# Kernel optimization log

Hardware: AMD Instinct MI355X
Metric: run time of the kernel (lower is better)

## Reference

```python
import jax, jax.numpy as jnp
import numpy as np

H_SIZE = 128
E_SIZE = 16
N_LAYERS = 3
N_ATOMS = 80000
N_BLOCKS = 16000
N_EDGES = 320000
N_GRAPHS = 128


def setup_inputs() -> dict:
    key = jax.random.key(0)
    ks = jax.random.split(key, 20)
    p = lambda k, shape: (0.02 * jax.random.normal(k, shape, dtype=jnp.float32))
    h = H_SIZE
    inp = {
        'H': jax.random.normal(ks[0], (N_ATOMS, h), dtype=jnp.float32),
        'Z': jax.random.normal(ks[1], (N_ATOMS, 1, 3), dtype=jnp.float32),
        'block_id': jnp.sort(jax.random.randint(ks[2], (N_ATOMS,), 0, N_BLOCKS)),
        'batch_id': jnp.sort(jax.random.randint(ks[3], (N_BLOCKS,), 0, N_GRAPHS)),
        'edges': jax.random.randint(ks[4], (2, N_EDGES), 0, N_BLOCKS),
        'edge_attr': jax.random.normal(ks[5], (N_EDGES, E_SIZE), dtype=jnp.float32),
        # EGNN parameters
        'emb_in_w': p(ks[6], (h, h)), 'emb_in_b': jnp.zeros((h,), jnp.float32),
        'emb_out_w': p(ks[7], (h, h)), 'emb_out_b': jnp.zeros((h,), jnp.float32),
        'edge_w1': p(ks[8], (N_LAYERS, 2 * h + 1 + E_SIZE, h)), 'edge_b1': jnp.zeros((N_LAYERS, h), jnp.float32),
        'edge_w2': p(ks[9], (N_LAYERS, h, h)), 'edge_b2': jnp.zeros((N_LAYERS, h), jnp.float32),
        'node_w1': p(ks[10], (N_LAYERS, 2 * h, h)), 'node_b1': jnp.zeros((N_LAYERS, h), jnp.float32),
        'node_w2': p(ks[11], (N_LAYERS, h, h)), 'node_b2': jnp.zeros((N_LAYERS, h), jnp.float32),
        'coord_w1': p(ks[12], (N_LAYERS, h, h)), 'coord_b1': jnp.zeros((N_LAYERS, h), jnp.float32),
        'coord_w3': p(ks[13], (N_LAYERS, h, 1)),  # final coord layer, no bias
    }
    return inp


def _normalize(x, eps=1e-12):
    # F.normalize(dim=-1): x / max(||x||_2, eps)
    n = jnp.linalg.norm(x, axis=-1, keepdims=True)
    return x / jnp.maximum(n, eps)


def _seg_mean(x, ids, n):
    s = jax.ops.segment_sum(x, ids, num_segments=n)
    c = jax.ops.segment_sum(jnp.ones((x.shape[0], 1), x.dtype), ids, num_segments=n)
    return s / jnp.maximum(c, 1.0)


def _egnn_forward(H, Z, block_id, batch_id, edges, edge_attr,
                  emb_in_w, emb_in_b, emb_out_w, emb_out_b,
                  edge_w1, edge_b1, edge_w2, edge_b2,
                  node_w1, node_b1, node_w2, node_b2,
                  coord_w1, coord_b1, coord_w3):
    silu = jax.nn.silu
    # atom -> block pooling (scatter_mean)
    Hm = _seg_mean(H, block_id, N_BLOCKS)                      # [B, h]
    x = _seg_mean(Z.reshape(Z.shape[0], -1), block_id, N_BLOCKS)  # [B, 3] (squeeze of [B,1,3])
    row, col = edges[0], edges[1]

    h = Hm @ emb_in_w + emb_in_b
    for l in range(N_LAYERS):
        diff = x[row] - x[col]                                 # [E, 3]
        radial = jnp.sum(diff * diff, axis=-1, keepdims=True)  # [E, 1]
        e_in = jnp.concatenate([h[row], h[col], radial, edge_attr], axis=-1)  # [E, 2h+1+e]
        m = silu(silu(e_in @ edge_w1[l] + edge_b1[l]) @ edge_w2[l] + edge_b2[l])  # edge MLP [E, h]
        # coordinate update: per-edge scalar weight, mean aggregation
        w = silu(m @ coord_w1[l] + coord_b1[l]) @ coord_w3[l]  # [E, 1]
        x = x + _seg_mean(diff * w, row, N_BLOCKS)
        # node update: sum aggregation of messages, residual
        agg = jax.ops.segment_sum(m, row, num_segments=N_BLOCKS)  # [B, h]
        h = h + (silu(jnp.concatenate([h, agg], axis=-1) @ node_w1[l] + node_b1[l]) @ node_w2[l] + node_b2[l])
    h = h @ emb_out_w + emb_out_b

    block_repr = _normalize(h)                                  # [B, h]
    graph_repr = _normalize(jax.ops.segment_sum(block_repr, batch_id, num_segments=N_GRAPHS))  # [G, h]
    return Hm, block_repr, graph_repr


def reference(H, Z, block_id, batch_id, edges, edge_attr,
              emb_in_w, emb_in_b, emb_out_w, emb_out_b,
              edge_w1, edge_b1, edge_w2, edge_b2,
              node_w1, node_b1, node_w2, node_b2,
              coord_w1, coord_b1, coord_w3):
    return _egnn_forward(H, Z, block_id, batch_id, edges, edge_attr,
                         emb_in_w, emb_in_b, emb_out_w, emb_out_b,
                         edge_w1, edge_b1, edge_w2, edge_b2,
                         node_w1, node_b1, node_w2, node_b2,
                         coord_w1, coord_b1, coord_w3)
```

## Files before the change

### kernel.cpp

```cpp
#include <hip/hip_runtime.h>

#define N_ATOMS  80000
#define N_BLOCKS 16000
#define N_EDGES  320000
#define N_GRAPHS 128
#define HS       128

typedef unsigned short ushortT;
typedef __attribute__((ext_vector_type(8))) __bf16 bf16x8;
typedef __attribute__((ext_vector_type(8))) unsigned short ushort8;
typedef __attribute__((ext_vector_type(4))) float f32x4;

__device__ __forceinline__ unsigned short f2bf(float f){
  unsigned int u = __builtin_bit_cast(unsigned int, f);
  u = (u + 0x7FFFu + ((u >> 16) & 1u)) >> 16;
  return (unsigned short)u;
}
__device__ __forceinline__ ushortT f2bff(float f){
  __bf16 b = (__bf16)f;
  return __builtin_bit_cast(ushortT, b);
}
__device__ __forceinline__ float bf2f(ushortT u){
  unsigned int v = ((unsigned int)u) << 16;
  return __builtin_bit_cast(float, v);
}
__device__ __forceinline__ bf16x8 load8bf(const ushortT* p){
  uint4 u = *reinterpret_cast<const uint4*>(p);
  return __builtin_bit_cast(bf16x8, u);
}
__device__ __forceinline__ bf16x8 load8f_bf(const float* p){
  float4 a = *reinterpret_cast<const float4*>(p);
  float4 b = *reinterpret_cast<const float4*>(p + 4);
  ushort8 u = { f2bff(a.x), f2bff(a.y), f2bff(a.z), f2bff(a.w),
                f2bff(b.x), f2bff(b.y), f2bff(b.z), f2bff(b.w) };
  return __builtin_bit_cast(bf16x8, u);
}
__device__ __forceinline__ float silu(float v){
  return v * __builtin_amdgcn_rcpf(1.f + __expf(-v));
}

__device__ __forceinline__ int c_of_p(int p){
  int ks = p >> 5, lg = (p >> 3) & 3, j = p & 7;
  return 16 * (ks * 2 + (j >> 2)) + lg * 4 + (j & 3);
}

struct PrepParams {
  const float* ew1; const float* ew2; const float* cw1;
  const float* nw1; const float* nw2; const float* ei; const float* eo;
  const float* eb1;
  ushortT* W1atp; ushortT* W1btp; ushortT* W1ct; ushortT* W2tp; ushortT* CW1tp;
  ushortT* NW1t; ushortT* NW2t; ushortT* Eint; ushortT* Eoutt;
  float* b1p; int* hist;
};

__device__ __forceinline__ void tcvt(int idx, const float* __restrict__ src,
                                     ushortT* __restrict__ dst,
                                     int srcK, int row_off, int K, int N, int Kpad,
                                     int pn, int pk){
  int k = idx % Kpad;
  int rem = idx / Kpad;
  int n = rem % N;
  int l = rem / N;
  float v = 0.f;
  if (k < K){
    int kk = pk ? c_of_p(k) : k;
    int nn = pn ? c_of_p(n) : n;
    v = src[((size_t)l * srcK + row_off + kk) * N + nn];
  }
  dst[idx] = f2bf(v);
}

#define PREP_TOTAL (49152*5 + 12288 + 98304 + 16384*2 + 16000 + 384)

__global__ void prep_kernel(PrepParams P){
  int idx = blockIdx.x * 256 + threadIdx.x;
  if (idx < 49152){ tcvt(idx, P.ew1, P.W1atp, 273,   0, 128, 128, 128, 1, 0); return; }
  idx -= 49152;
  if (idx < 49152){ tcvt(idx, P.ew1, P.W1btp, 273, 128, 128, 128, 128, 1, 0); return; }
  idx -= 49152;
  if (idx < 12288){ tcvt(idx, P.ew1, P.W1ct,  273, 256,  17, 128,  32, 0, 0); return; }
  idx -= 12288;
  if (idx < 49152){ tcvt(idx, P.ew2, P.W2tp,  128,   0, 128, 128, 128, 0, 1); return; }
  idx -= 49152;
  if (idx < 49152){ tcvt(idx, P.cw1, P.CW1tp, 128,   0, 128, 128, 128, 0, 1); return; }
  idx -= 49152;
  if (idx < 98304){ tcvt(idx, P.nw1, P.NW1t,  256,   0, 256, 128, 256, 0, 0); return; }
  idx -= 98304;
  if (idx < 49152){ tcvt(idx, P.nw2, P.NW2t,  128,   0, 128, 128, 128, 0, 0); return; }
  idx -= 49152;
  if (idx < 16384){ tcvt(idx, P.ei,  P.Eint,  128,   0, 128, 128, 128, 0, 0); return; }
  idx -= 16384;
  if (idx < 16384){ tcvt(idx, P.eo,  P.Eoutt, 128,   0, 128, 128, 128, 0, 0); return; }
  idx -= 16384;
  if (idx < 16000){ P.hist[idx] = 0; return; }
  idx -= 16000;
  if (idx < 384){ int l = idx >> 7, p = idx & 127; P.b1p[idx] = P.eb1[l * 128 + c_of_p(p)]; }
}

__global__ void hist_bstart_kernel(const int* __restrict__ edges, int* __restrict__ hist,
                                   const int* __restrict__ bid, int* __restrict__ bstart){
  int b = blockIdx.x;
  if (b < N_EDGES / 256){
    int e = b * 256 + threadIdx.x;
    atomicAdd(&hist[edges[e]], 1);
  } else {
    int i = (b - N_EDGES / 256) * 256 + threadIdx.x;
    if (i <= N_BLOCKS){
      int lo = 0, hi = N_ATOMS;
      while (lo < hi){ int mid = (lo + hi) >> 1; if (bid[mid] < i) lo = mid + 1; else hi = mid; }
      bstart[i] = lo;
    }
  }
}

__global__ __launch_bounds__(1024) void scan_kernel(const int* __restrict__ hist,
                                                    int* __restrict__ estart,
                                                    int* __restrict__ ecur){
  __shared__ int ps[1024];
  int t = threadIdx.x;
  const int chunk = (N_BLOCKS + 1023) / 1024;
  int lo = t * chunk, hi = lo + chunk;
  if (hi > N_BLOCKS) hi = N_BLOCKS;
  if (lo > N_BLOCKS) lo = N_BLOCKS;
  int s = 0;
  for (int i = lo; i < hi; i++) s += hist[i];
  ps[t] = s;
  __syncthreads();
  for (int off = 1; off < 1024; off <<= 1){
    int v = (t >= off) ? ps[t - off] : 0;
    __syncthreads();
    ps[t] += v;
    __syncthreads();
  }
  int base = (t == 0) ? 0 : ps[t - 1];
  for (int i = lo; i < hi; i++){ estart[i] = base; ecur[i] = base; base += hist[i]; }
  if (t == 1023) estart[N_BLOCKS] = base;
}

__global__ void scatter_kernel(const int* __restrict__ edges, const float* __restrict__ attr,
                               int* __restrict__ ecur,
                               int* __restrict__ srow, int* __restrict__ scol,
                               ushortT* __restrict__ sattr){
  int e = blockIdx.x * 256 + threadIdx.x;
  if (e >= N_EDGES) return;
  int r = edges[e], c = edges[N_EDGES + e];
  int p = atomicAdd(&ecur[r], 1);
  srow[p] = r; scol[p] = c;
  ushortT buf[32];
  buf[0] = 0;
#pragma unroll
  for (int k = 0; k < 16; k++) buf[k + 1] = f2bf(attr[(size_t)e * 16 + k]);
#pragma unroll
  for (int k = 17; k < 32; k++) buf[k] = 0;
#pragma unroll
  for (int k = 0; k < 16; k++)
    reinterpret_cast<uint*>(sattr + (size_t)p * 32)[k] = reinterpret_cast<uint*>(buf)[k];
}

__global__ void pool_kernel(const float* __restrict__ H, const float* __restrict__ Z,
                            const int* __restrict__ start,
                            float* __restrict__ Hm, float* __restrict__ x,
                            float* __restrict__ gsum){
  int b = blockIdx.x;
  int t = threadIdx.x;
  if (b < 128) gsum[b * 128 + t] = 0.f;
  int s = start[b], e = start[b + 1];
  float inv = 1.f / (float)((e - s) > 0 ? (e - s) : 1);
  float sum = 0.f;
  for (int a = s; a < e; a++) sum += H[(size_t)a * HS + t];
  Hm[(size_t)b * HS + t] = sum * inv;
  if (t < 3){
    float sz = 0.f;
    for (int a = s; a < e; a++) sz += Z[a * 3 + t];
    x[b * 3 + t] = sz * inv;
  }
}

__global__ __launch_bounds__(64) void gemm_pq_kernel(
    const float* __restrict__ A,
    const ushortT* __restrict__ Wt, const float* __restrict__ bias,
    float* __restrict__ Cf,
    const ushortT* __restrict__ Wa, const ushortT* __restrict__ Wb,
    const float* __restrict__ b1p,
    ushortT* __restrict__ Pbf, ushortT* __restrict__ Qbf,
    float* __restrict__ agg, float* __restrict__ xacc){
  __shared__ __align__(16) ushortT T1[2048];
  int lane = threadIdx.x;
  int l15 = lane & 15, lg = lane >> 4;
  int base = blockIdx.x * 16;
  int row = base + l15;
  {
    float4 z4 = {0.f, 0.f, 0.f, 0.f};
    float4* aggp = reinterpret_cast<float4*>(agg + (size_t)blockIdx.x * 16 * HS);
#pragma unroll
    for (int i = 0; i < 8; i++) aggp[lane + 64 * i] = z4;
    if (lane < 48) xacc[blockIdx.x * 48 + lane] = 0.f;
  }
  f32x4 zero = {0.f, 0.f, 0.f, 0.f};
  f32x4 acc[8];
#pragma unroll
  for (int n = 0; n < 8; n++) acc[n] = zero;
#pragma unroll
  for (int ks = 0; ks < 4; ks++){
    int k0 = ks * 32 + lg * 8;
    bf16x8 af = load8f_bf(A + (size_t)row * HS + k0);
#pragma unroll
    for (int n = 0; n < 8; n++){
      bf16x8 bf = load8bf(Wt + (size_t)(16 * n + l15) * HS + k0);
      acc[n] = __builtin_amdgcn_mfma_f32_16x16x32_bf16(af, bf, acc[n], 0, 0, 0);
    }
  }
#pragma unroll
  for (int n = 0; n < 8; n++){
    int col = 16 * n + l15;
    float bv = bias[col];
#pragma unroll
    for (int r = 0; r < 4; r++){
      int ro = base + lg * 4 + r;
      int er = lg * 4 + r;
      float hv = acc[n][r] + bv;
      Cf[(size_t)ro * HS + col] = hv;
      T1[(er * 128 + col) ^ ((er & 7) << 3)] = f2bff(hv);
    }
  }
  f32x4 accp[8], accq[8];
#pragma unroll
  for (int n = 0; n < 8; n++){ accp[n] = zero; accq[n] = zero; }
#pragma unroll
  for (int ks = 0; ks < 4; ks++){
    int k0 = ks * 32 + lg * 8;
    bf16x8 af = load8bf(&T1[(l15 * 128 + k0) ^ ((l15 & 7) << 3)]);
#pragma unroll
    for (int n = 0; n < 8; n++){
      accp[n] = __builtin_amdgcn_mfma_f32_16x16x32_bf16(af, load8bf(Wa + (size_t)(16 * n + l15) * HS + k0), accp[n], 0, 0, 0);
      accq[n] = __builtin_amdgcn_mfma_f32_16x16x32_bf16(af, load8bf(Wb + (size_t)(16 * n + l15) * HS + k0), accq[n], 0, 0, 0);
    }
  }
#pragma unroll
  for (int n = 0; n < 8; n++){
    int col = 16 * n + l15;
    float bv = b1p[col];
#pragma unroll
    for (int r = 0; r < 4; r++){
      int ro = base + lg * 4 + r;
      Pbf[(size_t)ro * HS + col] = f2bff(accp[n][r] + bv);
      Qbf[(size_t)ro * HS + col] = f2bff(accq[n][r]);
    }
  }
}

__global__ __launch_bounds__(64) void node_pq_kernel(
    float* __restrict__ h, float* __restrict__ agg,
    const ushortT* __restrict__ W1t, const ushortT* __restrict__ W2t,
    const float* __restrict__ b1, const float* __restrict__ b2,
    const ushortT* __restrict__ Wa, const ushortT* __restrict__ Wb,
    const float* __restrict__ b1p,
    ushortT* __restrict__ Pbf, ushortT* __restrict__ Qbf,
    float* __restrict__ x, float* __restrict__ xacc, const int* __restrict__ estart){
  __shared__ __align__(16) ushortT T1[2048];
  int lane = threadIdx.x;
  int l15 = lane & 15, lg = lane >> 4;
  int base = blockIdx.x * 16;
  int row = base + l15;
  f32x4 zero = {0.f, 0.f, 0.f, 0.f};

  if (lane < 48){
    int i = blockIdx.x * 48 + lane;
    int b = i / 3;
    int cnt = estart[b + 1] - estart[b];
    x[i] += xacc[i] / (float)(cnt > 0 ? cnt : 1);
    xacc[i] = 0.f;
  }

  f32x4 acc[8];
#pragma unroll
  for (int n = 0; n < 8; n++) acc[n] = zero;
#pragma unroll
  for (int ks = 0; ks < 8; ks++){
    int k0 = ks * 32 + lg * 8;
    bf16x8 af = (k0 < 128) ? load8f_bf(h + (size_t)row * HS + k0)
                           : load8f_bf(agg + (size_t)row * HS + (k0 - 128));
#pragma unroll
    for (int n = 0; n < 8; n++){
      acc[n] = __builtin_amdgcn_mfma_f32_16x16x32_bf16(af, load8bf(W1t + (size_t)(16 * n + l15) * 256 + k0), acc[n], 0, 0, 0);
    }
  }
  __syncthreads();
  {
    float4 z4 = {0.f, 0.f, 0.f, 0.f};
    float4* aggp = reinterpret_cast<float4*>(agg + (size_t)blockIdx.x * 16 * HS);
#pragma unroll
    for (int i = 0; i < 8; i++) aggp[lane + 64 * i] = z4;
  }
#pragma unroll
  for (int n = 0; n < 8; n++){
    int col = 16 * n + l15;
    float bv = b1[col];
#pragma unroll
    for (int r = 0; r < 4; r++){
      int er = lg * 4 + r;
      T1[(er * 128 + col) ^ ((er & 7) << 3)] = f2bff(silu(acc[n][r] + bv));
    }
  }
#pragma unroll
  for (int n = 0; n < 8; n++) acc[n] = zero;
#pragma unroll
  for (int ks = 0; ks < 4; ks++){
    int k0 = ks * 32 + lg * 8;
    bf16x8 af = load8bf(&T1[(l15 * 128 + k0) ^ ((l15 & 7) << 3)]);
#pragma unroll
    for (int n = 0; n < 8; n++){
      acc[n] = __builtin_amdgcn_mfma_f32_16x16x32_bf16(af, load8bf(W2t + (size_t)(16 * n + l15) * HS + k0), acc[n], 0, 0, 0);
    }
  }
#pragma unroll
  for (int n = 0; n < 8; n++){
    int col = 16 * n + l15;
    float bv = b2[col];
#pragma unroll
    for (int r = 0; r < 4; r++){
      int ro = base + lg * 4 + r;
      int er = lg * 4 + r;
      float hv = h[(size_t)ro * HS + col] + acc[n][r] + bv;
      h[(size_t)ro * HS + col] = hv;
      T1[(er * 128 + col) ^ ((er & 7) << 3)] = f2bff(hv);
    }
  }
  f32x4 accp[8], accq[8];
#pragma unroll
  for (int n = 0; n < 8; n++){ accp[n] = zero; accq[n] = zero; }
#pragma unroll
  for (int ks = 0; ks < 4; ks++){
    int k0 = ks * 32 + lg * 8;
    bf16x8 af = load8bf(&T1[(l15 * 128 + k0) ^ ((l15 & 7) << 3)]);
#pragma unroll
    for (int n = 0; n < 8; n++){
      accp[n] = __builtin_amdgcn_mfma_f32_16x16x32_bf16(af, load8bf(Wa + (size_t)(16 * n + l15) * HS + k0), accp[n], 0, 0, 0);
      accq[n] = __builtin_amdgcn_mfma_f32_16x16x32_bf16(af, load8bf(Wb + (size_t)(16 * n + l15) * HS + k0), accq[n], 0, 0, 0);
    }
  }
#pragma unroll
  for (int n = 0; n < 8; n++){
    int col = 16 * n + l15;
    float bv = b1p[col];
#pragma unroll
    for (int r = 0; r < 4; r++){
      int ro = base + lg * 4 + r;
      Pbf[(size_t)ro * HS + col] = f2bff(accp[n][r] + bv);
      Qbf[(size_t)ro * HS + col] = f2bff(accq[n][r]);
    }
  }
}

__global__ __launch_bounds__(64) void node_emb_kernel(
    const float* __restrict__ h, const float* __restrict__ agg,
    const ushortT* __restrict__ W1t, const ushortT* __restrict__ W2t,
    const float* __restrict__ b1, const float* __restrict__ b2,
    const ushortT* __restrict__ Eoutt, const float* __restrict__ eob,
    const int* __restrict__ batch_id,
    float* __restrict__ brep, float* __restrict__ gsum){
  __shared__ __align__(16) ushortT T1[2048];
  int lane = threadIdx.x;
  int l15 = lane & 15, lg = lane >> 4;
  int base = blockIdx.x * 16;
  int row = base + l15;
  f32x4 zero = {0.f, 0.f, 0.f, 0.f};

  f32x4 acc[8];
#pragma unroll
  for (int n = 0; n < 8; n++) acc[n] = zero;
#pragma unroll
  for (int ks = 0; ks < 8; ks++){
    int k0 = ks * 32 + lg * 8;
    bf16x8 af = (k0 < 128) ? load8f_bf(h + (size_t)row * HS + k0)
                           : load8f_bf(agg + (size_t)row * HS + (k0 - 128));
#pragma unroll
    for (int n = 0; n < 8; n++){
      acc[n] = __builtin_amdgcn_mfma_f32_16x16x32_bf16(af, load8bf(W1t + (size_t)(16 * n + l15) * 256 + k0), acc[n], 0, 0, 0);
    }
  }
#pragma unroll
  for (int n = 0; n < 8; n++){
    int col = 16 * n + l15;
    float bv = b1[col];
#pragma unroll
    for (int r = 0; r < 4; r++){
      int er = lg * 4 + r;
      T1[(er * 128 + col) ^ ((er & 7) << 3)] = f2bff(silu(acc[n][r] + bv));
    }
  }
#pragma unroll
  for (int n = 0; n < 8; n++) acc[n] = zero;
#pragma unroll
  for (int ks = 0; ks < 4; ks++){
    int k0 = ks * 32 + lg * 8;
    bf16x8 af = load8bf(&T1[(l15 * 128 + k0) ^ ((l15 & 7) << 3)]);
#pragma unroll
    for (int n = 0; n < 8; n++){
      acc[n] = __builtin_amdgcn_mfma_f32_16x16x32_bf16(af, load8bf(W2t + (size_t)(16 * n + l15) * HS + k0), acc[n], 0, 0, 0);
    }
  }
#pragma unroll
  for (int n = 0; n < 8; n++){
    int col = 16 * n + l15;
    float bv = b2[col];
#pragma unroll
    for (int r = 0; r < 4; r++){
      int ro = base + lg * 4 + r;
      int er = lg * 4 + r;
      float hv = h[(size_t)ro * HS + col] + acc[n][r] + bv;
      T1[(er * 128 + col) ^ ((er & 7) << 3)] = f2bff(hv);
    }
  }
#pragma unroll
  for (int n = 0; n < 8; n++) acc[n] = zero;
#pragma unroll
  for (int ks = 0; ks < 4; ks++){
    int k0 = ks * 32 + lg * 8;
    bf16x8 af = load8bf(&T1[(l15 * 128 + k0) ^ ((l15 & 7) << 3)]);
#pragma unroll
    for (int n = 0; n < 8; n++){
      acc[n] = __builtin_amdgcn_mfma_f32_16x16x32_bf16(af, load8bf(Eoutt + (size_t)(16 * n + l15) * HS + k0), acc[n], 0, 0, 0);
    }
  }
#pragma unroll
  for (int n = 0; n < 8; n++){
    float bv = eob[16 * n + l15];
#pragma unroll
    for (int r = 0; r < 4; r++) acc[n][r] += bv;
  }
  float scl[4];
#pragma unroll
  for (int r = 0; r < 4; r++){
    float ss = 0.f;
#pragma unroll
    for (int n = 0; n < 8; n++) ss += acc[n][r] * acc[n][r];
#pragma unroll
    for (int o = 1; o < 16; o <<= 1) ss += __shfl_xor(ss, o, 64);
    scl[r] = 1.f / fmaxf(sqrtf(ss), 1e-12f);
  }
#pragma unroll
  for (int r = 0; r < 4; r++){
    int ro = base + lg * 4 + r;
    int g = batch_id[ro];
#pragma unroll
    for (int n = 0; n < 8; n++){
      int col = 16 * n + l15;
      float v = acc[n][r] * scl[r];
      brep[(size_t)ro * HS + col] = v;
      atomicAdd(&gsum[g * HS + col], v);
    }
  }
}

template<int COORD>
__global__ __launch_bounds__(256, 4) void edge_kernel(
    const int* __restrict__ srow, const int* __restrict__ scol,
    const ushortT* __restrict__ sattr,
    const float* __restrict__ x,
    const ushortT* __restrict__ Pbf, const ushortT* __restrict__ Qbf,
    const ushortT* __restrict__ W1ct, const ushortT* __restrict__ W2tp,
    const ushortT* __restrict__ CW1tp,
    const float* __restrict__ b2, const float* __restrict__ cb1,
    const float* __restrict__ cw3,
    float* __restrict__ xacc, float* __restrict__ agg){
  __shared__ float bias_l[3][128];
  __shared__ int   rid_s[64];
  __shared__ float dif_s[COORD ? 64 : 1][3];
  __shared__ float wall[COORD ? 4 : 1][COORD ? 64 : 1];
  __shared__ __align__(16) ushortT S1[64 * 128];
  __shared__ __align__(16) ushortT S2[64 * 128];

  const int t = threadIdx.x;
  const int lane = t & 63;
  const int wv = t >> 6;
  const int l15 = lane & 15, lg = lane >> 4;
  const f32x4 zero = {0.f, 0.f, 0.f, 0.f};

  if (t < 128){
    bias_l[0][t] = b2[t];
    if (COORD){ bias_l[1][t] = cb1[t]; bias_l[2][t] = cw3[t]; }
  }

  const int erow = wv * 16 + l15;
  const int e = blockIdx.x * 64 + erow;
  const int r = srow[e], c = scol[e];
  const float dx = x[r * 3 + 0] - x[c * 3 + 0];
  const float dy = x[r * 3 + 1] - x[c * 3 + 1];
  const float dz = x[r * 3 + 2] - x[c * 3 + 2];
  const float rad = dx * dx + dy * dy + dz * dz;
  if (lg == 0){
    rid_s[erow] = r;
    if (COORD){ dif_s[erow][0] = dx; dif_s[erow][1] = dy; dif_s[erow][2] = dz; }
  }
  ushort8 at8 = __builtin_bit_cast(ushort8, load8bf(sattr + (size_t)e * 32 + lg * 8));
  if (lg == 0) at8[0] = f2bff(rad);
  const bf16x8 atb = __builtin_bit_cast(bf16x8, at8);

#pragma unroll
  for (int ks = 0; ks < 4; ks++){
    f32x4 a0 = __builtin_amdgcn_mfma_f32_16x16x32_bf16(
        load8bf(W1ct + (size_t)(16 * (2 * ks)     + l15) * 32 + lg * 8), atb, zero, 0, 0, 0);
    f32x4 a1 = __builtin_amdgcn_mfma_f32_16x16x32_bf16(
        load8bf(W1ct + (size_t)(16 * (2 * ks + 1) + l15) * 32 + lg * 8), atb, zero, 0, 0, 0);
    ushort8 pv = __builtin_bit_cast(ushort8, load8bf(Pbf + (size_t)r * HS + ks * 32 + lg * 8));
    ushort8 qv = __builtin_bit_cast(ushort8, load8bf(Qbf + (size_t)c * HS + ks * 32 + lg * 8));
    ushort8 af;
#pragma unroll
    for (int j = 0; j < 4; j++)
      af[j] = f2bff(silu(a0[j] + bf2f(pv[j]) + bf2f(qv[j])));
#pragma unroll
    for (int j = 4; j < 8; j++)
      af[j] = f2bff(silu(a1[j - 4] + bf2f(pv[j]) + bf2f(qv[j])));
    int byte = (erow * 256 + ks * 64 + lg * 16) ^ ((erow & 7) << 4);
    *reinterpret_cast<uint4*>(reinterpret_cast<char*>(S1) + byte) = __builtin_bit_cast(uint4, af);
  }
  __syncthreads();

  f32x4 acc2[4][2];
#pragma unroll
  for (int et = 0; et < 4; et++){ acc2[et][0] = zero; acc2[et][1] = zero; }
#pragma unroll
  for (int ks = 0; ks < 4; ks++){
    bf16x8 wf0 = load8bf(W2tp + (size_t)(16 * (2 * wv)     + l15) * HS + ks * 32 + lg * 8);
    bf16x8 wf1 = load8bf(W2tp + (size_t)(16 * (2 * wv + 1) + l15) * HS + ks * 32 + lg * 8);
#pragma unroll
    for (int et = 0; et < 4; et++){
      int row2 = et * 16 + l15;
      int byte = (row2 * 256 + ks * 64 + lg * 16) ^ ((row2 & 7) << 4);
      bf16x8 mb = __builtin_bit_cast(bf16x8,
          *reinterpret_cast<const uint4*>(reinterpret_cast<const char*>(S1) + byte));
      acc2[et][0] = __builtin_amdgcn_mfma_f32_16x16x32_bf16(wf0, mb, acc2[et][0], 0, 0, 0);
      acc2[et][1] = __builtin_amdgcn_mfma_f32_16x16x32_bf16(wf1, mb, acc2[et][1], 0, 0, 0);
    }
  }
  ushort8 mreg[4];
#pragma unroll
  for (int et = 0; et < 4; et++){
    ushort8 mq;
#pragma unroll
    for (int g = 0; g < 2; g++){
      float4 bv = *reinterpret_cast<const float4*>(&bias_l[0][16 * (2 * wv + g) + lg * 4]);
#pragma unroll
      for (int rr = 0; rr < 4; rr++)
        mq[g * 4 + rr] = f2bff(silu(acc2[et][g][rr] + (&bv.x)[rr]));
    }
    mreg[et] = mq;
    int row2 = et * 16 + l15;
    int byte = (row2 * 256 + wv * 64 + lg * 16) ^ ((row2 & 7) << 4);
    *reinterpret_cast<uint4*>(reinterpret_cast<char*>(S2) + byte) = __builtin_bit_cast(uint4, mq);
  }
  __syncthreads();

  if (COORD){
    f32x4 acc3[4][2];
#pragma unroll
    for (int et = 0; et < 4; et++){ acc3[et][0] = zero; acc3[et][1] = zero; }
#pragma unroll
    for (int ks = 0; ks < 4; ks++){
      bf16x8 wf0 = load8bf(CW1tp + (size_t)(16 * (2 * wv)     + l15) * HS + ks * 32 + lg * 8);
      bf16x8 wf1 = load8bf(CW1tp + (size_t)(16 * (2 * wv + 1) + l15) * HS + ks * 32 + lg * 8);
#pragma unroll
      for (int et = 0; et < 4; et++){
        bf16x8 mb;
        if (ks == wv){
          mb = __builtin_bit_cast(bf16x8, mreg[et]);
        } else {
          int row2 = et * 16 + l15;
          int byte = (row2 * 256 + ks * 64 + lg * 16) ^ ((row2 & 7) << 4);
          mb = __builtin_bit_cast(bf16x8,
              *reinterpret_cast<const uint4*>(reinterpret_cast<const char*>(S2) + byte));
        }
        acc3[et][0] = __builtin_amdgcn_mfma_f32_16x16x32_bf16(wf0, mb, acc3[et][0], 0, 0, 0);
        acc3[et][1] = __builtin_amdgcn_mfma_f32_16x16x32_bf16(wf1, mb, acc3[et][1], 0, 0, 0);
      }
    }
#pragma unroll
    for (int et = 0; et < 4; et++){
      float ws = 0.f;
#pragma unroll
      for (int g = 0; g < 2; g++){
        int n = 2 * wv + g;
        float4 cbv = *reinterpret_cast<const float4*>(&bias_l[1][16 * n + lg * 4]);
        float4 cwv = *reinterpret_cast<const float4*>(&bias_l[2][16 * n + lg * 4]);
#pragma unroll
        for (int rr = 0; rr < 4; rr++)
          ws += silu(acc3[et][g][rr] + (&cbv.x)[rr]) * (&cwv.x)[rr];
      }
      ws += __shfl_xor(ws, 16, 64);
      ws += __shfl_xor(ws, 32, 64);
      if (lg == 0) wall[wv][et * 16 + l15] = ws;
    }
  }

  {
    const int c0 = c_of_p(2 * lane), c1 = c_of_p(2 * lane + 1);
    float run0 = 0.f, run1 = 0.f;
    int prev = __builtin_amdgcn_readfirstlane(rid_s[wv * 16]);
#pragma unroll
    for (int e2 = 0; e2 < 16; e2++){
      int re = __builtin_amdgcn_readfirstlane(rid_s[wv * 16 + e2]);
      if (re != prev){
        atomicAdd(&agg[(size_t)prev * HS + c0], run0);
        atomicAdd(&agg[(size_t)prev * HS + c1], run1);
        run0 = 0.f; run1 = 0.f; prev = re;
      }
      int row2 = wv * 16 + e2;
      int byte = (row2 * 256 + lane * 4) ^ ((row2 & 7) << 4);
      uint u = *reinterpret_cast<const uint*>(reinterpret_cast<const char*>(S2) + byte);
      run0 += bf2f((ushortT)(u & 0xFFFF));
      run1 += bf2f((ushortT)(u >> 16));
    }
    atomicAdd(&agg[(size_t)prev * HS + c0], run0);
    atomicAdd(&agg[(size_t)prev * HS + c1], run1);
  }

  if (COORD){
    __syncthreads();
    if (t < 192){
      int e2 = t / 3, cd = t % 3;
      float w = wall[0][e2] + wall[1][e2] + wall[2][e2] + wall[3][e2];
      atomicAdd(&xacc[(size_t)rid_s[e2] * 3 + cd], dif_s[e2][cd] * w);
    }
  }
}

__global__ void norm_graph_kernel(const float* __restrict__ gsum, float* __restrict__ grep){
  int wv = threadIdx.x >> 6, lane = threadIdx.x & 63;
  int g = blockIdx.x * 4 + wv;
  if (g >= N_GRAPHS) return;
  float v0 = gsum[g * HS + lane];
  float v1 = gsum[g * HS + 64 + lane];
  float ss = v0 * v0 + v1 * v1;
#pragma unroll
  for (int o = 1; o < 64; o <<= 1) ss += __shfl_xor(ss, o, 64);
  float s = 1.f / fmaxf(sqrtf(ss), 1e-12f);
  grep[(size_t)g * HS + lane] = v0 * s;
  grep[(size_t)g * HS + 64 + lane] = v1 * s;
}

extern "C" void kernel_launch(void* const* d_in, const int* in_sizes, int n_in,
                              void* d_out, int out_size, void* d_ws, size_t ws_size,
                              hipStream_t stream){
  const float* H         = (const float*)d_in[0];
  const float* Z         = (const float*)d_in[1];
  const int*   block_id  = (const int*)d_in[2];
  const int*   batch_id  = (const int*)d_in[3];
  const int*   edges     = (const int*)d_in[4];
  const float* edge_attr = (const float*)d_in[5];
  const float* emb_in_w  = (const float*)d_in[6];
  const float* emb_in_b  = (const float*)d_in[7];
  const float* emb_out_w = (const float*)d_in[8];
  const float* emb_out_b = (const float*)d_in[9];
  const float* edge_w1   = (const float*)d_in[10];
  const float* edge_b1   = (const float*)d_in[11];
  const float* edge_w2   = (const float*)d_in[12];
  const float* edge_b2   = (const float*)d_in[13];
  const float* node_w1   = (const float*)d_in[14];
  const float* node_b1   = (const float*)d_in[15];
  const float* node_w2   = (const float*)d_in[16];
  const float* node_b2   = (const float*)d_in[17];
  const float* coord_w1  = (const float*)d_in[18];
  const float* coord_b1  = (const float*)d_in[19];
  const float* coord_w3  = (const float*)d_in[20];

  float* out  = (float*)d_out;
  float* Hm   = out;
  float* brep = out + (size_t)N_BLOCKS * HS;
  float* grep = out + (size_t)2 * N_BLOCKS * HS;

  char* base = (char*)d_ws;
  size_t off = 0;
  auto take = [&](size_t bytes) -> char* {
    char* p = base + off;
    off += (bytes + 255) & ~(size_t)255;
    return p;
  };
  float*   x     = (float*)  take((size_t)N_BLOCKS * 3 * 4);
  float*   xacc  = (float*)  take((size_t)N_BLOCKS * 3 * 4);
  float*   h     = (float*)  take((size_t)N_BLOCKS * HS * 4);
  float*   agg   = (float*)  take((size_t)N_BLOCKS * HS * 4);
  float*   gsum  = (float*)  take((size_t)N_GRAPHS * HS * 4);
  int*     bstart= (int*)    take((size_t)(N_BLOCKS + 1) * 4);
  int*     hist  = (int*)    take((size_t)N_BLOCKS * 4);
  int*     estart= (int*)    take((size_t)(N_BLOCKS + 1) * 4);
  int*     ecur  = (int*)    take((size_t)N_BLOCKS * 4);
  int*     srow  = (int*)    take((size_t)N_EDGES * 4);
  int*     scol  = (int*)    take((size_t)N_EDGES * 4);
  ushortT* sattr = (ushortT*)take((size_t)N_EDGES * 32 * 2);
  ushortT* Pbf   = (ushortT*)take((size_t)N_BLOCKS * HS * 2);
  ushortT* Qbf   = (ushortT*)take((size_t)N_BLOCKS * HS * 2);
  ushortT* W1atp = (ushortT*)take((size_t)3 * 128 * 128 * 2);
  ushortT* W1btp = (ushortT*)take((size_t)3 * 128 * 128 * 2);
  ushortT* W1ct  = (ushortT*)take((size_t)3 * 128 * 32 * 2);
  ushortT* W2tp  = (ushortT*)take((size_t)3 * 128 * 128 * 2);
  ushortT* CW1tp = (ushortT*)take((size_t)3 * 128 * 128 * 2);
  ushortT* NW1t  = (ushortT*)take((size_t)3 * 128 * 256 * 2);
  ushortT* NW2t  = (ushortT*)take((size_t)3 * 128 * 128 * 2);
  ushortT* Eint  = (ushortT*)take((size_t)128 * 128 * 2);
  ushortT* Eoutt = (ushortT*)take((size_t)128 * 128 * 2);
  float*   b1p   = (float*)  take((size_t)3 * 128 * 4);

  PrepParams P;
  P.ew1 = edge_w1; P.ew2 = edge_w2; P.cw1 = coord_w1;
  P.nw1 = node_w1; P.nw2 = node_w2; P.ei = emb_in_w; P.eo = emb_out_w;
  P.eb1 = edge_b1;
  P.W1atp = W1atp; P.W1btp = W1btp; P.W1ct = W1ct; P.W2tp = W2tp; P.CW1tp = CW1tp;
  P.NW1t = NW1t; P.NW2t = NW2t; P.Eint = Eint; P.Eoutt = Eoutt;
  P.b1p = b1p; P.hist = hist;
  prep_kernel<<<(PREP_TOTAL + 255) / 256, 256, 0, stream>>>(P);

  hist_bstart_kernel<<<N_EDGES / 256 + (N_BLOCKS + 1 + 255) / 256, 256, 0, stream>>>(
      edges, hist, block_id, bstart);
  scan_kernel<<<1, 1024, 0, stream>>>(hist, estart, ecur);
  scatter_kernel<<<N_EDGES / 256, 256, 0, stream>>>(edges, edge_attr, ecur, srow, scol, sattr);
  pool_kernel<<<N_BLOCKS, 128, 0, stream>>>(H, Z, bstart, Hm, x, gsum);

  gemm_pq_kernel<<<N_BLOCKS / 16, 64, 0, stream>>>(Hm, Eint, emb_in_b, h,
                                                   W1atp, W1btp, b1p, Pbf, Qbf, agg, xacc);

  for (int l = 0; l < 3; l++){
    if (l < 2){
      edge_kernel<1><<<N_EDGES / 64, 256, 0, stream>>>(
          srow, scol, sattr, x, Pbf, Qbf,
          W1ct + (size_t)l * 128 * 32, W2tp + (size_t)l * 128 * 128, CW1tp + (size_t)l * 128 * 128,
          edge_b2 + l * 128, coord_b1 + l * 128, coord_w3 + l * 128,
          xacc, agg);
      node_pq_kernel<<<N_BLOCKS / 16, 64, 0, stream>>>(
          h, agg, NW1t + (size_t)l * 128 * 256, NW2t + (size_t)l * 128 * 128,
          node_b1 + l * 128, node_b2 + l * 128,
          W1atp + (size_t)(l + 1) * 128 * 128, W1btp + (size_t)(l + 1) * 128 * 128,
          b1p + (l + 1) * 128, Pbf, Qbf, x, xacc, estart);
    } else {
      edge_kernel<0><<<N_EDGES / 64, 256, 0, stream>>>(
          srow, scol, sattr, x, Pbf, Qbf,
          W1ct + (size_t)l * 128 * 32, W2tp + (size_t)l * 128 * 128, CW1tp + (size_t)l * 128 * 128,
          edge_b2 + l * 128, coord_b1 + l * 128, coord_w3 + l * 128,
          xacc, agg);
      node_emb_kernel<<<N_BLOCKS / 16, 64, 0, stream>>>(
          h, agg, NW1t + (size_t)l * 128 * 256, NW2t + (size_t)l * 128 * 128,
          node_b1 + l * 128, node_b2 + l * 128,
          Eoutt, emb_out_b, batch_id, brep, gsum);
    }
  }

  norm_graph_kernel<<<N_GRAPHS / 4, 256, 0, stream>>>(gsum, grep);
}
```

Measured before the change: 521.5 us.

## Process two edge tiles per block, reusing weight fragments in registers

```diff
diff --git a/kernel.cpp b/kernel.cpp
--- a/kernel.cpp
+++ b/kernel.cpp
@@ -454,7 +454,7 @@
 }
 
 template<int COORD>
-__global__ __launch_bounds__(256, 4) void edge_kernel(
+__global__ __launch_bounds__(256, 3) void edge_kernel(
     const int* __restrict__ srow, const int* __restrict__ scol,
     const ushortT* __restrict__ sattr,
     const float* __restrict__ x,
@@ -482,146 +482,162 @@
     if (COORD){ bias_l[1][t] = cb1[t]; bias_l[2][t] = cw3[t]; }
   }
 
+  bf16x8 wf2[4][2];
+  bf16x8 cwf[4][2];
+  const int c0 = c_of_p(2 * lane), c1 = c_of_p(2 * lane + 1);
+  float run0 = 0.f, run1 = 0.f;
+  int prev = -1;
+
   const int erow = wv * 16 + l15;
-  const int e = blockIdx.x * 64 + erow;
-  const int r = srow[e], c = scol[e];
-  const float dx = x[r * 3 + 0] - x[c * 3 + 0];
-  const float dy = x[r * 3 + 1] - x[c * 3 + 1];
-  const float dz = x[r * 3 + 2] - x[c * 3 + 2];
-  const float rad = dx * dx + dy * dy + dz * dz;
-  if (lg == 0){
-    rid_s[erow] = r;
-    if (COORD){ dif_s[erow][0] = dx; dif_s[erow][1] = dy; dif_s[erow][2] = dz; }
-  }
-  ushort8 at8 = __builtin_bit_cast(ushort8, load8bf(sattr + (size_t)e * 32 + lg * 8));
-  if (lg == 0) at8[0] = f2bff(rad);
-  const bf16x8 atb = __builtin_bit_cast(bf16x8, at8);
-
-#pragma unroll
-  for (int ks = 0; ks < 4; ks++){
-    f32x4 a0 = __builtin_amdgcn_mfma_f32_16x16x32_bf16(
-        load8bf(W1ct + (size_t)(16 * (2 * ks)     + l15) * 32 + lg * 8), atb, zero, 0, 0, 0);
-    f32x4 a1 = __builtin_amdgcn_mfma_f32_16x16x32_bf16(
-        load8bf(W1ct + (size_t)(16 * (2 * ks + 1) + l15) * 32 + lg * 8), atb, zero, 0, 0, 0);
-    ushort8 pv = __builtin_bit_cast(ushort8, load8bf(Pbf + (size_t)r * HS + ks * 32 + lg * 8));
-    ushort8 qv = __builtin_bit_cast(ushort8, load8bf(Qbf + (size_t)c * HS + ks * 32 + lg * 8));
-    ushort8 af;
-#pragma unroll
-    for (int j = 0; j < 4; j++)
-      af[j] = f2bff(silu(a0[j] + bf2f(pv[j]) + bf2f(qv[j])));
-#pragma unroll
-    for (int j = 4; j < 8; j++)
-      af[j] = f2bff(silu(a1[j - 4] + bf2f(pv[j]) + bf2f(qv[j])));
-    int byte = (erow * 256 + ks * 64 + lg * 16) ^ ((erow & 7) << 4);
-    *reinterpret_cast<uint4*>(reinterpret_cast<char*>(S1) + byte) = __builtin_bit_cast(uint4, af);
-  }
-  __syncthreads();
-
-  f32x4 acc2[4][2];
-#pragma unroll
-  for (int et = 0; et < 4; et++){ acc2[et][0] = zero; acc2[et][1] = zero; }
-#pragma unroll
-  for (int ks = 0; ks < 4; ks++){
-    bf16x8 wf0 = load8bf(W2tp + (size_t)(16 * (2 * wv)     + l15) * HS + ks * 32 + lg * 8);
-    bf16x8 wf1 = load8bf(W2tp + (size_t)(16 * (2 * wv + 1) + l15) * HS + ks * 32 + lg * 8);
+
+#pragma unroll
+  for (int tile = 0; tile < 2; tile++){
+    const int e = blockIdx.x * 128 + tile * 64 + erow;
+    const int r = srow[e], c = scol[e];
+    const float dx = x[r * 3 + 0] - x[c * 3 + 0];
+    const float dy = x[r * 3 + 1] - x[c * 3 + 1];
+    const float dz = x[r * 3 + 2] - x[c * 3 + 2];
+    const float rad = dx * dx + dy * dy + dz * dz;
+    ushort8 at8 = __builtin_bit_cast(ushort8, load8bf(sattr + (size_t)e * 32 + lg * 8));
+    if (lg == 0) at8[0] = f2bff(rad);
+    const bf16x8 atb = __builtin_bit_cast(bf16x8, at8);
+
+#pragma unroll
+    for (int ks = 0; ks < 4; ks++){
+      f32x4 a0 = __builtin_amdgcn_mfma_f32_16x16x32_bf16(
+          load8bf(W1ct + (size_t)(16 * (2 * ks)     + l15) * 32 + lg * 8), atb, zero, 0, 0, 0);
+      f32x4 a1 = __builtin_amdgcn_mfma_f32_16x16x32_bf16(
+          load8bf(W1ct + (size_t)(16 * (2 * ks + 1) + l15) * 32 + lg * 8), atb, zero, 0, 0, 0);
+      ushort8 pv = __builtin_bit_cast(ushort8, load8bf(Pbf + (size_t)r * HS + ks * 32 + lg * 8));
+      ushort8 qv = __builtin_bit_cast(ushort8, load8bf(Qbf + (size_t)c * HS + ks * 32 + lg * 8));
+      ushort8 af;
+#pragma unroll
+      for (int j = 0; j < 4; j++)
+        af[j] = f2bff(silu(a0[j] + bf2f(pv[j]) + bf2f(qv[j])));
+#pragma unroll
+      for (int j = 4; j < 8; j++)
+        af[j] = f2bff(silu(a1[j - 4] + bf2f(pv[j]) + bf2f(qv[j])));
+      int byte = (erow * 256 + ks * 64 + lg * 16) ^ ((erow & 7) << 4);
+      *reinterpret_cast<uint4*>(reinterpret_cast<char*>(S1) + byte) = __builtin_bit_cast(uint4, af);
+    }
+    __syncthreads();
+
+    if (lg == 0){
+      rid_s[erow] = r;
+      if (COORD){ dif_s[erow][0] = dx; dif_s[erow][1] = dy; dif_s[erow][2] = dz; }
+    }
+
+    f32x4 acc2[4][2];
+#pragma unroll
+    for (int et = 0; et < 4; et++){ acc2[et][0] = zero; acc2[et][1] = zero; }
+#pragma unroll
+    for (int ks = 0; ks < 4; ks++){
+      if (tile == 0){
+        wf2[ks][0] = load8bf(W2tp + (size_t)(16 * (2 * wv)     + l15) * HS + ks * 32 + lg * 8);
+        wf2[ks][1] = load8bf(W2tp + (size_t)(16 * (2 * wv + 1) + l15) * HS + ks * 32 + lg * 8);
+      }
+#pragma unroll
+      for (int et = 0; et < 4; et++){
+        int row2 = et * 16 + l15;
+        int byte = (row2 * 256 + ks * 64 + lg * 16) ^ ((row2 & 7) << 4);
+        bf16x8 mb = __builtin_bit_cast(bf16x8,
+            *reinterpret_cast<const uint4*>(reinterpret_cast<const char*>(S1) + byte));
+        acc2[et][0] = __builtin_amdgcn_mfma_f32_16x16x32_bf16(wf2[ks][0], mb, acc2[et][0], 0, 0, 0);
+        acc2[et][1] = __builtin_amdgcn_mfma_f32_16x16x32_bf16(wf2[ks][1], mb, acc2[et][1], 0, 0, 0);
+      }
+    }
+    ushort8 mreg[4];
 #pragma unroll
     for (int et = 0; et < 4; et++){
+      ushort8 mq;
+#pragma unroll
+      for (int g = 0; g < 2; g++){
+        float4 bv = *reinterpret_cast<const float4*>(&bias_l[0][16 * (2 * wv + g) + lg * 4]);
+#pragma unroll
+        for (int rr = 0; rr < 4; rr++)
+          mq[g * 4 + rr] = f2bff(silu(acc2[et][g][rr] + (&bv.x)[rr]));
+      }
+      mreg[et] = mq;
       int row2 = et * 16 + l15;
-      int byte = (row2 * 256 + ks * 64 + lg * 16) ^ ((row2 & 7) << 4);
-      bf16x8 mb = __builtin_bit_cast(bf16x8,
-          *reinterpret_cast<const uint4*>(reinterpret_cast<const char*>(S1) + byte));
-      acc2[et][0] = __builtin_amdgcn_mfma_f32_16x16x32_bf16(wf0, mb, acc2[et][0], 0, 0, 0);
-      acc2[et][1] = __builtin_amdgcn_mfma_f32_16x16x32_bf16(wf1, mb, acc2[et][1], 0, 0, 0);
-    }
-  }
-  ushort8 mreg[4];
-#pragma unroll
-  for (int et = 0; et < 4; et++){
-    ushort8 mq;
-#pragma unroll
-    for (int g = 0; g < 2; g++){
-      float4 bv = *reinterpret_cast<const float4*>(&bias_l[0][16 * (2 * wv + g) + lg * 4]);
-#pragma unroll
-      for (int rr = 0; rr < 4; rr++)
-        mq[g * 4 + rr] = f2bff(silu(acc2[et][g][rr] + (&bv.x)[rr]));
-    }
-    mreg[et] = mq;
-    int row2 = et * 16 + l15;
-    int byte = (row2 * 256 + wv * 64 + lg * 16) ^ ((row2 & 7) << 4);
-    *reinterpret_cast<uint4*>(reinterpret_cast<char*>(S2) + byte) = __builtin_bit_cast(uint4, mq);
-  }
-  __syncthreads();
-
-  if (COORD){
-    f32x4 acc3[4][2];
-#pragma unroll
-    for (int et = 0; et < 4; et++){ acc3[et][0] = zero; acc3[et][1] = zero; }
-#pragma unroll
-    for (int ks = 0; ks < 4; ks++){
-      bf16x8 wf0 = load8bf(CW1tp + (size_t)(16 * (2 * wv)     + l15) * HS + ks * 32 + lg * 8);
-      bf16x8 wf1 = load8bf(CW1tp + (size_t)(16 * (2 * wv + 1) + l15) * HS + ks * 32 + lg * 8);
+      int byte = (row2 * 256 + wv * 64 + lg * 16) ^ ((row2 & 7) << 4);
+      *reinterpret_cast<uint4*>(reinterpret_cast<char*>(S2) + byte) = __builtin_bit_cast(uint4, mq);
+    }
+    __syncthreads();
+
+    if (COORD){
+      f32x4 acc3[4][2];
+#pragma unroll
+      for (int et = 0; et < 4; et++){ acc3[et][0] = zero; acc3[et][1] = zero; }
+#pragma unroll
+      for (int ks = 0; ks < 4; ks++){
+        if (tile == 0){
+          cwf[ks][0] = load8bf(CW1tp + (size_t)(16 * (2 * wv)     + l15) * HS + ks * 32 + lg * 8);
+          cwf[ks][1] = load8bf(CW1tp + (size_t)(16 * (2 * wv + 1) + l15) * HS + ks * 32 + lg * 8);
+        }
+#pragma unroll
+        for (int et = 0; et < 4; et++){
+          bf16x8 mb;
+          if (ks == wv){
+            mb = __builtin_bit_cast(bf16x8, mreg[et]);
+          } else {
+            int row2 = et * 16 + l15;
+            int byte = (row2 * 256 + ks * 64 + lg * 16) ^ ((row2 & 7) << 4);
+            mb = __builtin_bit_cast(bf16x8,
+                *reinterpret_cast<const uint4*>(reinterpret_cast<const char*>(S2) + byte));
+          }
+          acc3[et][0] = __builtin_amdgcn_mfma_f32_16x16x32_bf16(cwf[ks][0], mb, acc3[et][0], 0, 0, 0);
+          acc3[et][1] = __builtin_amdgcn_mfma_f32_16x16x32_bf16(cwf[ks][1], mb, acc3[et][1], 0, 0, 0);
+        }
+      }
 #pragma unroll
       for (int et = 0; et < 4; et++){
-        bf16x8 mb;
-        if (ks == wv){
-          mb = __builtin_bit_cast(bf16x8, mreg[et]);
-        } else {
-          int row2 = et * 16 + l15;
-          int byte = (row2 * 256 + ks * 64 + lg * 16) ^ ((row2 & 7) << 4);
-          mb = __builtin_bit_cast(bf16x8,
-              *reinterpret_cast<const uint4*>(reinterpret_cast<const char*>(S2) + byte));
+        float ws = 0.f;
+#pragma unroll
+        for (int g = 0; g < 2; g++){
+          int n = 2 * wv + g;
+          float4 cbv = *reinterpret_cast<const float4*>(&bias_l[1][16 * n + lg * 4]);
+          float4 cwv = *reinterpret_cast<const float4*>(&bias_l[2][16 * n + lg * 4]);
+#pragma unroll
+          for (int rr = 0; rr < 4; rr++)
+            ws += silu(acc3[et][g][rr] + (&cbv.x)[rr]) * (&cwv.x)[rr];
         }
-        acc3[et][0] = __builtin_amdgcn_mfma_f32_16x16x32_bf16(wf0, mb, acc3[et][0], 0, 0, 0);
-        acc3[et][1] = __builtin_amdgcn_mfma_f32_16x16x32_bf16(wf1, mb, acc3[et][1], 0, 0, 0);
+        ws += __shfl_xor(ws, 16, 64);
+        ws += __shfl_xor(ws, 32, 64);
+        if (lg == 0) wall[wv][et * 16 + l15] = ws;
       }
     }
-#pragma unroll
-    for (int et = 0; et < 4; et++){
-      float ws = 0.f;
-#pragma unroll
-      for (int g = 0; g < 2; g++){
-        int n = 2 * wv + g;
-        float4 cbv = *reinterpret_cast<const float4*>(&bias_l[1][16 * n + lg * 4]);
-        float4 cwv = *reinterpret_cast<const float4*>(&bias_l[2][16 * n + lg * 4]);
-#pragma unroll
-        for (int rr = 0; rr < 4; rr++)
-          ws += silu(acc3[et][g][rr] + (&cbv.x)[rr]) * (&cwv.x)[rr];
+
+    {
+#pragma unroll
+      for (int e2 = 0; e2 < 16; e2++){
+        int re = __builtin_amdgcn_readfirstlane(rid_s[wv * 16 + e2]);
+        if (re != prev){
+          if (prev >= 0){
+            atomicAdd(&agg[(size_t)prev * HS + c0], run0);
+            atomicAdd(&agg[(size_t)prev * HS + c1], run1);
+          }
+          run0 = 0.f; run1 = 0.f; prev = re;
+        }
+        int row2 = wv * 16 + e2;
+        int byte = (row2 * 256 + lane * 4) ^ ((row2 & 7) << 4);
+        uint u = *reinterpret_cast<const uint*>(reinterpret_cast<const char*>(S2) + byte);
+        run0 += bf2f((ushortT)(u & 0xFFFF));
+        run1 += bf2f((ushortT)(u >> 16));
       }
-      ws += __shfl_xor(ws, 16, 64);
-      ws += __shfl_xor(ws, 32, 64);
-      if (lg == 0) wall[wv][et * 16 + l15] = ws;
-    }
-  }
-
-  {
-    const int c0 = c_of_p(2 * lane), c1 = c_of_p(2 * lane + 1);
-    float run0 = 0.f, run1 = 0.f;
-    int prev = __builtin_amdgcn_readfirstlane(rid_s[wv * 16]);
-#pragma unroll
-    for (int e2 = 0; e2 < 16; e2++){
-      int re = __builtin_amdgcn_readfirstlane(rid_s[wv * 16 + e2]);
-      if (re != prev){
-        atomicAdd(&agg[(size_t)prev * HS + c0], run0);
-        atomicAdd(&agg[(size_t)prev * HS + c1], run1);
-        run0 = 0.f; run1 = 0.f; prev = re;
+    }
+
+    if (COORD){
+      __syncthreads();
+      if (t < 192){
+        int e2 = t / 3, cd = t % 3;
+        float w = wall[0][e2] + wall[1][e2] + wall[2][e2] + wall[3][e2];
+        atomicAdd(&xacc[(size_t)rid_s[e2] * 3 + cd], dif_s[e2][cd] * w);
       }
-      int row2 = wv * 16 + e2;
-      int byte = (row2 * 256 + lane * 4) ^ ((row2 & 7) << 4);
-      uint u = *reinterpret_cast<const uint*>(reinterpret_cast<const char*>(S2) + byte);
-      run0 += bf2f((ushortT)(u & 0xFFFF));
-      run1 += bf2f((ushortT)(u >> 16));
-    }
+    }
+  }
+  if (prev >= 0){
     atomicAdd(&agg[(size_t)prev * HS + c0], run0);
     atomicAdd(&agg[(size_t)prev * HS + c1], run1);
-  }
-
-  if (COORD){
-    __syncthreads();
-    if (t < 192){
-      int e2 = t / 3, cd = t % 3;
-      float w = wall[0][e2] + wall[1][e2] + wall[2][e2] + wall[3][e2];
-      atomicAdd(&xacc[(size_t)rid_s[e2] * 3 + cd], dif_s[e2][cd] * w);
-    }
   }
 }
 
@@ -721,7 +737,7 @@
 
   for (int l = 0; l < 3; l++){
     if (l < 2){
-      edge_kernel<1><<<N_EDGES / 64, 256, 0, stream>>>(
+      edge_kernel<1><<<N_EDGES / 128, 256, 0, stream>>>(
           srow, scol, sattr, x, Pbf, Qbf,
           W1ct + (size_t)l * 128 * 32, W2tp + (size_t)l * 128 * 128, CW1tp + (size_t)l * 128 * 128,
           edge_b2 + l * 128, coord_b1 + l * 128, coord_w3 + l * 128,
@@ -732,7 +748,7 @@
           W1atp + (size_t)(l + 1) * 128 * 128, W1btp + (size_t)(l + 1) * 128 * 128,
           b1p + (l + 1) * 128, Pbf, Qbf, x, xacc, estart);
     } else {
-      edge_kernel<0><<<N_EDGES / 64, 256, 0, stream>>>(
+      edge_kernel<0><<<N_EDGES / 128, 256, 0, stream>>>(
           srow, scol, sattr, x, Pbf, Qbf,
           W1ct + (size_t)l * 128 * 32, W2tp + (size_t)l * 128 * 128, CW1tp + (size_t)l * 128 * 128,
           edge_b2 + l * 128, coord_b1 + l * 128, coord_w3 + l * 128,
```

Result: slower. 542.0 us (+3.9%).

## Process 128 edges per block with 8 waves each owning one output column tile

Applied to the files above, without the earlier changes.

```diff
diff --git a/kernel.cpp b/kernel.cpp
--- a/kernel.cpp
+++ b/kernel.cpp
@@ -454,7 +454,7 @@
 }
 
 template<int COORD>
-__global__ __launch_bounds__(256, 4) void edge_kernel(
+__global__ __launch_bounds__(512, 2) void edge_kernel(
     const int* __restrict__ srow, const int* __restrict__ scol,
     const ushortT* __restrict__ sattr,
     const float* __restrict__ x,
@@ -465,11 +465,11 @@
     const float* __restrict__ cw3,
     float* __restrict__ xacc, float* __restrict__ agg){
   __shared__ float bias_l[3][128];
-  __shared__ int   rid_s[64];
-  __shared__ float dif_s[COORD ? 64 : 1][3];
-  __shared__ float wall[COORD ? 4 : 1][COORD ? 64 : 1];
-  __shared__ __align__(16) ushortT S1[64 * 128];
-  __shared__ __align__(16) ushortT S2[64 * 128];
+  __shared__ int   rid_s[128];
+  __shared__ float dif_s[COORD ? 128 : 1][3];
+  __shared__ float wall[COORD ? 8 : 1][COORD ? 128 : 1];
+  __shared__ __align__(16) ushortT S1[128 * 128];
+  __shared__ __align__(16) ushortT S2[128 * 128];
 
   const int t = threadIdx.x;
   const int lane = t & 63;
@@ -483,7 +483,7 @@
   }
 
   const int erow = wv * 16 + l15;
-  const int e = blockIdx.x * 64 + erow;
+  const int e = blockIdx.x * 128 + erow;
   const int r = srow[e], c = scol[e];
   const float dx = x[r * 3 + 0] - x[c * 3 + 0];
   const float dy = x[r * 3 + 1] - x[c * 3 + 1];
@@ -517,79 +517,67 @@
   }
   __syncthreads();
 
-  f32x4 acc2[4][2];
-#pragma unroll
-  for (int et = 0; et < 4; et++){ acc2[et][0] = zero; acc2[et][1] = zero; }
+  f32x4 acc2[8];
+#pragma unroll
+  for (int et = 0; et < 8; et++) acc2[et] = zero;
 #pragma unroll
   for (int ks = 0; ks < 4; ks++){
-    bf16x8 wf0 = load8bf(W2tp + (size_t)(16 * (2 * wv)     + l15) * HS + ks * 32 + lg * 8);
-    bf16x8 wf1 = load8bf(W2tp + (size_t)(16 * (2 * wv + 1) + l15) * HS + ks * 32 + lg * 8);
-#pragma unroll
-    for (int et = 0; et < 4; et++){
+    bf16x8 wf = load8bf(W2tp + (size_t)(16 * wv + l15) * HS + ks * 32 + lg * 8);
+#pragma unroll
+    for (int et = 0; et < 8; et++){
       int row2 = et * 16 + l15;
       int byte = (row2 * 256 + ks * 64 + lg * 16) ^ ((row2 & 7) << 4);
       bf16x8 mb = __builtin_bit_cast(bf16x8,
           *reinterpret_cast<const uint4*>(reinterpret_cast<const char*>(S1) + byte));
-      acc2[et][0] = __builtin_amdgcn_mfma_f32_16x16x32_bf16(wf0, mb, acc2[et][0], 0, 0, 0);
-      acc2[et][1] = __builtin_amdgcn_mfma_f32_16x16x32_bf16(wf1, mb, acc2[et][1], 0, 0, 0);
-    }
-  }
-  ushort8 mreg[4];
-#pragma unroll
-  for (int et = 0; et < 4; et++){
-    ushort8 mq;
-#pragma unroll
-    for (int g = 0; g < 2; g++){
-      float4 bv = *reinterpret_cast<const float4*>(&bias_l[0][16 * (2 * wv + g) + lg * 4]);
+      acc2[et] = __builtin_amdgcn_mfma_f32_16x16x32_bf16(wf, mb, acc2[et], 0, 0, 0);
+    }
+  }
+  {
+    float4 bv = *reinterpret_cast<const float4*>(&bias_l[0][16 * wv + lg * 4]);
+    int pbyte = ((wv >> 1) * 32 + lg * 8 + (wv & 1) * 4) * 2;
+#pragma unroll
+    for (int et = 0; et < 8; et++){
+      ushortT mm[4];
 #pragma unroll
       for (int rr = 0; rr < 4; rr++)
-        mq[g * 4 + rr] = f2bff(silu(acc2[et][g][rr] + (&bv.x)[rr]));
-    }
-    mreg[et] = mq;
-    int row2 = et * 16 + l15;
-    int byte = (row2 * 256 + wv * 64 + lg * 16) ^ ((row2 & 7) << 4);
-    *reinterpret_cast<uint4*>(reinterpret_cast<char*>(S2) + byte) = __builtin_bit_cast(uint4, mq);
+        mm[rr] = f2bff(silu(acc2[et][rr] + (&bv.x)[rr]));
+      int row2 = et * 16 + l15;
+      int byte = (row2 * 256 + pbyte) ^ ((row2 & 7) << 4);
+      *reinterpret_cast<uint2*>(reinterpret_cast<char*>(S2) + byte) =
+          *reinterpret_cast<uint2*>(mm);
+    }
   }
   __syncthreads();
 
   if (COORD){
-    f32x4 acc3[4][2];
-#pragma unroll
-    for (int et = 0; et < 4; et++){ acc3[et][0] = zero; acc3[et][1] = zero; }
+    f32x4 acc3[8];
+#pragma unroll
+    for (int et = 0; et < 8; et++) acc3[et] = zero;
 #pragma unroll
     for (int ks = 0; ks < 4; ks++){
-      bf16x8 wf0 = load8bf(CW1tp + (size_t)(16 * (2 * wv)     + l15) * HS + ks * 32 + lg * 8);
-      bf16x8 wf1 = load8bf(CW1tp + (size_t)(16 * (2 * wv + 1) + l15) * HS + ks * 32 + lg * 8);
-#pragma unroll
-      for (int et = 0; et < 4; et++){
-        bf16x8 mb;
-        if (ks == wv){
-          mb = __builtin_bit_cast(bf16x8, mreg[et]);
-        } else {
-          int row2 = et * 16 + l15;
-          int byte = (row2 * 256 + ks * 64 + lg * 16) ^ ((row2 & 7) << 4);
-          mb = __builtin_bit_cast(bf16x8,
-              *reinterpret_cast<const uint4*>(reinterpret_cast<const char*>(S2) + byte));
-        }
-        acc3[et][0] = __builtin_amdgcn_mfma_f32_16x16x32_bf16(wf0, mb, acc3[et][0], 0, 0, 0);
-        acc3[et][1] = __builtin_amdgcn_mfma_f32_16x16x32_bf16(wf1, mb, acc3[et][1], 0, 0, 0);
+      bf16x8 wf = load8bf(CW1tp + (size_t)(16 * wv + l15) * HS + ks * 32 + lg * 8);
+#pragma unroll
+      for (int et = 0; et < 8; et++){
+        int row2 = et * 16 + l15;
+        int byte = (row2 * 256 + ks * 64 + lg * 16) ^ ((row2 & 7) << 4);
+        bf16x8 mb = __builtin_bit_cast(bf16x8,
+            *reinterpret_cast<const uint4*>(reinterpret_cast<const char*>(S2) + byte));
+        acc3[et] = __builtin_amdgcn_mfma_f32_16x16x32_bf16(wf, mb, acc3[et], 0, 0, 0);
       }
     }
-#pragma unroll
-    for (int et = 0; et < 4; et++){
-      float ws = 0.f;
-#pragma unroll
-      for (int g = 0; g < 2; g++){
-        int n = 2 * wv + g;
-        float4 cbv = *reinterpret_cast<const float4*>(&bias_l[1][16 * n + lg * 4]);
-        float4 cwv = *reinterpret_cast<const float4*>(&bias_l[2][16 * n + lg * 4]);
+    {
+      float4 cbv = *reinterpret_cast<const float4*>(&bias_l[1][16 * wv + lg * 4]);
+      float4 cwv = *reinterpret_cast<const float4*>(&bias_l[2][16 * wv + lg * 4]);
+#pragma unroll
+      for (int et = 0; et < 8; et++){
+        float ws = 0.f;
 #pragma unroll
         for (int rr = 0; rr < 4; rr++)
-          ws += silu(acc3[et][g][rr] + (&cbv.x)[rr]) * (&cwv.x)[rr];
+          ws += silu(acc3[et][rr] + (&cbv.x)[rr]) * (&cwv.x)[rr];
+        ws += __shfl_xor(ws, 16, 64);
+        ws += __shfl_xor(ws, 32, 64);
+        if (lg == 0) wall[wv][et * 16 + l15] = ws;
       }
-      ws += __shfl_xor(ws, 16, 64);
-      ws += __shfl_xor(ws, 32, 64);
-      if (lg == 0) wall[wv][et * 16 + l15] = ws;
     }
   }
 
@@ -617,9 +605,11 @@
 
   if (COORD){
     __syncthreads();
-    if (t < 192){
+    if (t < 384){
       int e2 = t / 3, cd = t % 3;
-      float w = wall[0][e2] + wall[1][e2] + wall[2][e2] + wall[3][e2];
+      float w = 0.f;
+#pragma unroll
+      for (int wv2 = 0; wv2 < 8; wv2++) w += wall[wv2][e2];
       atomicAdd(&xacc[(size_t)rid_s[e2] * 3 + cd], dif_s[e2][cd] * w);
     }
   }
@@ -721,7 +711,7 @@
 
   for (int l = 0; l < 3; l++){
     if (l < 2){
-      edge_kernel<1><<<N_EDGES / 64, 256, 0, stream>>>(
+      edge_kernel<1><<<N_EDGES / 128, 512, 0, stream>>>(
           srow, scol, sattr, x, Pbf, Qbf,
           W1ct + (size_t)l * 128 * 32, W2tp + (size_t)l * 128 * 128, CW1tp + (size_t)l * 128 * 128,
           edge_b2 + l * 128, coord_b1 + l * 128, coord_w3 + l * 128,
@@ -732,7 +722,7 @@
           W1atp + (size_t)(l + 1) * 128 * 128, W1btp + (size_t)(l + 1) * 128 * 128,
           b1p + (l + 1) * 128, Pbf, Qbf, x, xacc, estart);
     } else {
-      edge_kernel<0><<<N_EDGES / 64, 256, 0, stream>>>(
+      edge_kernel<0><<<N_EDGES / 128, 512, 0, stream>>>(
           srow, scol, sattr, x, Pbf, Qbf,
           W1ct + (size_t)l * 128 * 32, W2tp + (size_t)l * 128 * 128, CW1tp + (size_t)l * 128 * 128,
           edge_b2 + l * 128, coord_b1 + l * 128, coord_w3 + l * 128,
```

Result: faster. 505.0 us (-3.2%).
